# Performance work log

Hardware: AMD Instinct MI355X
Metric: run time of the kernel (lower is better)

The kernel has to match this reference:

```python
import jax, jax.numpy as jnp
import numpy as np

N_NODES = 100000


def setup_inputs() -> dict:
    key = jax.random.key(0)
    k1, k2, k3 = jax.random.split(key, 3)
    x = jax.random.normal(k1, (N_NODES, 256), dtype=jnp.float32)
    edge_index = jax.random.randint(k2, (2, 1600000), 0, N_NODES, dtype=jnp.int64)
    # GCNConv learned params (glorot weight, zero bias as in PyG init)
    W = jax.random.normal(k3, (256, 64), dtype=jnp.float32) * (1.0 / np.sqrt(256.0))
    b = jnp.zeros((64,), dtype=jnp.float32)
    return {"x": x, "edge_index": edge_index, "W": W, "b": b}


def reference(x, edge_index, W, b):
    n = x.shape[0]
    # --- gcn_norm: add self-loops, symmetric normalization ---
    loops = jnp.arange(n, dtype=edge_index.dtype)
    row = jnp.concatenate([edge_index[0], loops])  # source nodes
    col = jnp.concatenate([edge_index[1], loops])  # target nodes
    ones = jnp.ones(row.shape[0], dtype=x.dtype)
    deg = jax.ops.segment_sum(ones, col, num_segments=n)  # [N]
    dinv = jnp.where(deg > 0, jax.lax.rsqrt(deg), 0.0)
    norm = dinv[row] * dinv[col]  # [E+N]
    # --- linear transform then normalized scatter-add aggregation ---
    h = x @ W  # [N, out]
    msgs = h[row] * norm[:, None]  # [E+N, out]
    out = jax.ops.segment_sum(msgs, col, num_segments=n)  # [N, out]
    return out + b
```

## Files before the change

### kernel.cpp

```cpp
#include <hip/hip_runtime.h>


#define IN_F 256
#define OUT_F 64
#define WBITS 9
#define MAXBINS 256
#define CSHIFT 23
#define ROWMASK 0x7FFFFFu
#define CHUNK 4096

typedef unsigned short ushort_t;
typedef short bf16x8 __attribute__((ext_vector_type(8)));
typedef float f32x4 __attribute__((ext_vector_type(4)));

static __device__ __forceinline__ unsigned f2bf1(float f) {
    unsigned u = __float_as_uint(f);
    return (u + 0x7FFFu + ((u >> 16) & 1u)) >> 16;
}
static __device__ __forceinline__ unsigned pk2(float a, float b) {
    return f2bf1(a) | (f2bf1(b) << 16);
}
static __device__ __forceinline__ ushort_t f2bf(float f) { return (ushort_t)f2bf1(f); }
static __device__ __forceinline__ float bf2f(ushort_t h) {
    return __uint_as_float(((unsigned)h) << 16);
}

__global__ __launch_bounds__(256) void init_kernel(const float* __restrict__ W,
                                                   ushort_t* __restrict__ wfrag,
                                                   const int* __restrict__ col,
                                                   int* __restrict__ binCnt,
                                                   int* __restrict__ partialCnt,
                                                   int E, int nbins) {
    int gt = blockIdx.x * 256 + threadIdx.x;
    if (gt < 2048) {
        int t = gt;
        int kk = t >> 8;
        int ct = (t >> 6) & 3;
        int l  = t & 63;
        int k0 = kk * 32 + (l >> 4) * 8;
        int c  = ct * 16 + (l & 15);
        unsigned u0 = pk2(W[(k0 + 0) * OUT_F + c], W[(k0 + 1) * OUT_F + c]);
        unsigned u1 = pk2(W[(k0 + 2) * OUT_F + c], W[(k0 + 3) * OUT_F + c]);
        unsigned u2 = pk2(W[(k0 + 4) * OUT_F + c], W[(k0 + 5) * OUT_F + c]);
        unsigned u3 = pk2(W[(k0 + 6) * OUT_F + c], W[(k0 + 7) * OUT_F + c]);
        ((uint4*)wfrag)[t] = make_uint4(u0, u1, u2, u3);
    }
    __shared__ int hist[MAXBINS];
    int tid = threadIdx.x;
    if (tid < nbins) hist[tid] = 0;
    __syncthreads();
    int s = blockIdx.x * CHUNK;
    int epos = min(E, s + CHUNK);
    for (int e = s + tid; e < epos; e += 256)
        atomicAdd(&hist[col[e] >> WBITS], 1);
    __syncthreads();
    if (tid < nbins) {
        int c = hist[tid];
        partialCnt[blockIdx.x * MAXBINS + tid] = c;
        if (c) atomicAdd(&binCnt[tid], c);
    }
}

__global__ void bin_scan_kernel(const int* __restrict__ binCnt, int* __restrict__ binStart,
                                int* __restrict__ binCursor, int* __restrict__ start_n,
                                int nbins) {
    __shared__ int lds[MAXBINS];
    int tid = threadIdx.x;
    int v = (tid < nbins) ? binCnt[tid] : 0;
    lds[tid] = v;
    __syncthreads();
    for (int d = 1; d < MAXBINS; d <<= 1) {
        int t = (tid >= d) ? lds[tid - d] : 0;
        __syncthreads();
        lds[tid] += t;
        __syncthreads();
    }
    if (tid < nbins) {
        int ex = lds[tid] - v;
        binStart[tid] = ex;
        binCursor[tid] = ex;
    }
    if (tid == MAXBINS - 1) {
        binStart[nbins] = lds[MAXBINS - 1];
        start_n[0] = lds[MAXBINS - 1];
    }
}

__global__ __launch_bounds__(256) void mega_kernel(const float* __restrict__ x,
                                                   const ushort_t* __restrict__ wfrag,
                                                   ushort_t* __restrict__ h,
                                                   const int* __restrict__ row,
                                                   const int* __restrict__ col,
                                                   const int* __restrict__ partialCnt,
                                                   int* __restrict__ binCursor,
                                                   unsigned* __restrict__ ebuf,
                                                   int n, int E, int nbins, int gemmBlocks) {
    int tid = threadIdx.x;

    if (blockIdx.x < gemmBlocks) {
        int l  = tid & 63;
        int lr = l & 15;
        int lg = l >> 4;
        int rowbase = blockIdx.x * 64 + (tid >> 6) * 16;
        int arow = rowbase + lr;
        int lrow = (arow < n) ? arow : (n - 1);
        const float* xp = x + (size_t)lrow * IN_F + lg * 8;
        const uint4* wf = (const uint4*)wfrag;

        f32x4 acc0 = {0.f, 0.f, 0.f, 0.f};
        f32x4 acc1 = {0.f, 0.f, 0.f, 0.f};
        f32x4 acc2 = {0.f, 0.f, 0.f, 0.f};
        f32x4 acc3 = {0.f, 0.f, 0.f, 0.f};

        #pragma unroll
        for (int kk = 0; kk < 8; ++kk) {
            float4 xa = *(const float4*)(xp + kk * 32);
            float4 xb = *(const float4*)(xp + kk * 32 + 4);
            union { bf16x8 v; unsigned u[4]; } A;
            A.u[0] = pk2(xa.x, xa.y);
            A.u[1] = pk2(xa.z, xa.w);
            A.u[2] = pk2(xb.x, xb.y);
            A.u[3] = pk2(xb.z, xb.w);
            union { uint4 q; bf16x8 v; } B0, B1, B2, B3;
            B0.q = wf[(kk * 4 + 0) * 64 + l];
            B1.q = wf[(kk * 4 + 1) * 64 + l];
            B2.q = wf[(kk * 4 + 2) * 64 + l];
            B3.q = wf[(kk * 4 + 3) * 64 + l];
            acc0 = __builtin_amdgcn_mfma_f32_16x16x32_bf16(A.v, B0.v, acc0, 0, 0, 0);
            acc1 = __builtin_amdgcn_mfma_f32_16x16x32_bf16(A.v, B1.v, acc1, 0, 0, 0);
            acc2 = __builtin_amdgcn_mfma_f32_16x16x32_bf16(A.v, B2.v, acc2, 0, 0, 0);
            acc3 = __builtin_amdgcn_mfma_f32_16x16x32_bf16(A.v, B3.v, acc3, 0, 0, 0);
        }

        #pragma unroll
        for (int q = 0; q < 4; ++q) {
            int r = rowbase + lg * 4 + q;
            if (r < n) {
                ushort_t* gp = h + (size_t)r * OUT_F + lr;
                gp[0]  = f2bf(acc0[q]);
                gp[16] = f2bf(acc1[q]);
                gp[32] = f2bf(acc2[q]);
                gp[48] = f2bf(acc3[q]);
            }
        }
    } else {
        __shared__ int gbase[MAXBINS];
        __shared__ int lbase[MAXBINS];
        __shared__ int lcur[MAXBINS];
        __shared__ unsigned sorted[CHUNK];
        __shared__ int sdst[CHUNK];

        int sb = blockIdx.x - gemmBlocks;
        int s = sb * CHUNK;
        int epos = min(E, s + CHUNK);

        int c = (tid < nbins) ? partialCnt[sb * MAXBINS + tid] : 0;
        if (tid < nbins) gbase[tid] = c ? atomicAdd(&binCursor[tid], c) : 0;
        lbase[tid] = c;
        __syncthreads();
        for (int d = 1; d < MAXBINS; d <<= 1) {
            int t = (tid >= d) ? lbase[tid - d] : 0;
            __syncthreads();
            lbase[tid] += t;
            __syncthreads();
        }
        int ex = lbase[tid] - c;
        lbase[tid] = ex;
        lcur[tid] = ex;
        __syncthreads();

        for (int e = s + tid; e < epos; e += 256) {
            int cc = col[e];
            int bin = cc >> WBITS;
            int slot = atomicAdd(&lcur[bin], 1);
            sorted[slot] = (unsigned)row[e] | ((unsigned)(cc & ((1 << WBITS) - 1)) << CSHIFT);
            sdst[slot]   = gbase[bin] + (slot - lbase[bin]);
        }
        __syncthreads();

        int csize = epos - s;
        for (int i = tid; i < csize; i += 256)
            ebuf[sdst[i]] = sorted[i];
    }
}

__global__ __launch_bounds__(512) void fine_build_kernel(const unsigned* __restrict__ ebuf,
                                                         const int* __restrict__ binStart,
                                                         int* __restrict__ start,
                                                         float* __restrict__ dinv,
                                                         int* __restrict__ bucket, int n) {
    __shared__ int sdeg[512];
    __shared__ int scur[512];
    int b = blockIdx.x;
    int lo = b << WBITS;
    int wcnt = min(512, n - lo);
    int tid = threadIdx.x;
    sdeg[tid] = 0;
    __syncthreads();
    int s = binStart[b], epos = binStart[b + 1];
    for (int e = s + tid; e < epos; e += 512)
        atomicAdd(&sdeg[ebuf[e] >> CSHIFT], 1);
    __syncthreads();
    int d = sdeg[tid];
    if (tid < wcnt) dinv[lo + tid] = rsqrtf((float)(d + 1));
    for (int dd = 1; dd < 512; dd <<= 1) {
        int t = (tid >= dd) ? sdeg[tid - dd] : 0;
        __syncthreads();
        sdeg[tid] += t;
        __syncthreads();
    }
    int ex = sdeg[tid] - d;
    if (tid < wcnt) start[lo + tid] = s + ex;
    scur[tid] = ex;
    __syncthreads();
    for (int e = s + tid; e < epos; e += 512) {
        unsigned pr = ebuf[e];
        int pos = atomicAdd(&scur[pr >> CSHIFT], 1);
        bucket[s + pos] = (int)(pr & ROWMASK);
    }
}

__global__ __launch_bounds__(256) void gather_kernel(const int* __restrict__ start,
                              const int* __restrict__ bucket, const ushort_t* __restrict__ h,
                              const float* __restrict__ dinv, const float* __restrict__ b,
                              float* __restrict__ out, int n) {
    int lane = threadIdx.x & 63;
    int node = blockIdx.x * 4 + (threadIdx.x >> 6);
    if (node >= n) return;
    int f8  = lane & 7;
    int grp = lane >> 3;
    int s0  = start[node];
    int cnt = start[node + 1] - s0;
    const int* bp = bucket + s0;
    int last = cnt - 1;

    float a0 = 0.f, a1 = 0.f, a2 = 0.f, a3 = 0.f;
    float a4 = 0.f, a5 = 0.f, a6 = 0.f, a7 = 0.f;
    union { uint4 q; ushort_t s[8]; } VA, VB;
    for (int e0 = 0; e0 < cnt; e0 += 16) {
        int eA = e0 + grp;
        int eB = e0 + 8 + grp;
        int iA = bp[min(eA, last)];
        int iB = bp[min(eB, last)];
        VA.q = *(const uint4*)(h + (size_t)iA * OUT_F + f8 * 8);
        VB.q = *(const uint4*)(h + (size_t)iB * OUT_F + f8 * 8);
        float dA = (eA < cnt) ? dinv[iA] : 0.f;
        float dB = (eB < cnt) ? dinv[iB] : 0.f;
        a0 += bf2f(VA.s[0]) * dA;
        a1 += bf2f(VA.s[1]) * dA;
        a2 += bf2f(VA.s[2]) * dA;
        a3 += bf2f(VA.s[3]) * dA;
        a4 += bf2f(VA.s[4]) * dA;
        a5 += bf2f(VA.s[5]) * dA;
        a6 += bf2f(VA.s[6]) * dA;
        a7 += bf2f(VA.s[7]) * dA;
        a0 += bf2f(VB.s[0]) * dB;
        a1 += bf2f(VB.s[1]) * dB;
        a2 += bf2f(VB.s[2]) * dB;
        a3 += bf2f(VB.s[3]) * dB;
        a4 += bf2f(VB.s[4]) * dB;
        a5 += bf2f(VB.s[5]) * dB;
        a6 += bf2f(VB.s[6]) * dB;
        a7 += bf2f(VB.s[7]) * dB;
    }
    #pragma unroll
    for (int off = 8; off < 64; off <<= 1) {
        a0 += __shfl_xor(a0, off, 64);
        a1 += __shfl_xor(a1, off, 64);
        a2 += __shfl_xor(a2, off, 64);
        a3 += __shfl_xor(a3, off, 64);
        a4 += __shfl_xor(a4, off, 64);
        a5 += __shfl_xor(a5, off, 64);
        a6 += __shfl_xor(a6, off, 64);
        a7 += __shfl_xor(a7, off, 64);
    }

    if (grp == 0) {
        union { uint4 q; ushort_t s[8]; } SV;
        SV.q = *(const uint4*)(h + (size_t)node * OUT_F + f8 * 8);
        float dc = dinv[node];
        const float4* bv = (const float4*)b;
        float4 o0, o1;
        o0.x = (a0 + bf2f(SV.s[0]) * dc) * dc + bv[f8 * 2].x;
        o0.y = (a1 + bf2f(SV.s[1]) * dc) * dc + bv[f8 * 2].y;
        o0.z = (a2 + bf2f(SV.s[2]) * dc) * dc + bv[f8 * 2].z;
        o0.w = (a3 + bf2f(SV.s[3]) * dc) * dc + bv[f8 * 2].w;
        o1.x = (a4 + bf2f(SV.s[4]) * dc) * dc + bv[f8 * 2 + 1].x;
        o1.y = (a5 + bf2f(SV.s[5]) * dc) * dc + bv[f8 * 2 + 1].y;
        o1.z = (a6 + bf2f(SV.s[6]) * dc) * dc + bv[f8 * 2 + 1].z;
        o1.w = (a7 + bf2f(SV.s[7]) * dc) * dc + bv[f8 * 2 + 1].w;
        float4* op = (float4*)(out + (size_t)node * OUT_F + f8 * 8);
        op[0] = o0;
        op[1] = o1;
    }
}

extern "C" void kernel_launch(void* const* d_in, const int* in_sizes, int n_in,
                              void* d_out, int out_size, void* d_ws, size_t ws_size,
                              hipStream_t stream) {
    const float* x  = (const float*)d_in[0];
    const int*   ei = (const int*)d_in[1];
    const float* W  = (const float*)d_in[2];
    const float* b  = (const float*)d_in[3];
    float* out = (float*)d_out;

    int n = in_sizes[0] / IN_F;
    int E = in_sizes[1] / 2;
    const int* rowp = ei;
    const int* colp = ei + E;

    int nbins = (n + (1 << WBITS) - 1) >> WBITS;
    int SB = (E + CHUNK - 1) / CHUNK;

    char* wp = (char*)d_ws;
    ushort_t* h    = (ushort_t*)wp;
    unsigned* ebuf = (unsigned*)(wp + (size_t)n * OUT_F * 2);
    int* bucket    = (int*)(ebuf + E);
    ushort_t* wfrag = (ushort_t*)(bucket + E);
    int* start     = (int*)(wfrag + 16384);
    float* dinv    = (float*)(start + n + 1);
    int* binCnt    = (int*)(dinv + n);
    int* binStart  = binCnt + MAXBINS;
    int* binCursor = binStart + MAXBINS + 1;
    int* partialCnt= binCursor + MAXBINS;

    int gemmBlocks = (n + 63) / 64;

    hipMemsetAsync(binCnt, 0, MAXBINS * sizeof(int), stream);
    init_kernel<<<SB, 256, 0, stream>>>(W, wfrag, colp, binCnt, partialCnt, E, nbins);
    bin_scan_kernel<<<1, MAXBINS, 0, stream>>>(binCnt, binStart, binCursor, start + n, nbins);
    mega_kernel<<<gemmBlocks + SB, 256, 0, stream>>>(x, wfrag, h, rowp, colp,
                                                     partialCnt, binCursor, ebuf,
                                                     n, E, nbins, gemmBlocks);
    fine_build_kernel<<<nbins, 512, 0, stream>>>(ebuf, binStart, start, dinv, bucket, n);
    gather_kernel<<<(n + 3) / 4, 256, 0, stream>>>(start, bucket, h, dinv, b, out, n);
}
```

Before: 127.8 us.

## Pair GEMM with histogram pass and split scatter into its own kernel

The weight-fragment packing moves into a small standalone kernel. The GEMM blocks now share a launch with the column histogram instead of with the edge scatter, and the scatter runs as a separate kernel after the bin scan. The aim is to overlap the x@W GEMM with the lighter histogram pass and to give the scatter kernel leaner resources: its large LDS arrays are no longer shared with the GEMM code path, which may have limited occupancy. The cost is one extra kernel launch.

```diff
diff --git a/kernel.cpp b/kernel.cpp
--- a/kernel.cpp
+++ b/kernel.cpp
@@ -25,83 +25,52 @@
     return __uint_as_float(((unsigned)h) << 16);
 }
 
-__global__ __launch_bounds__(256) void init_kernel(const float* __restrict__ W,
-                                                   ushort_t* __restrict__ wfrag,
-                                                   const int* __restrict__ col,
-                                                   int* __restrict__ binCnt,
-                                                   int* __restrict__ partialCnt,
-                                                   int E, int nbins) {
-    int gt = blockIdx.x * 256 + threadIdx.x;
-    if (gt < 2048) {
-        int t = gt;
-        int kk = t >> 8;
-        int ct = (t >> 6) & 3;
-        int l  = t & 63;
-        int k0 = kk * 32 + (l >> 4) * 8;
-        int c  = ct * 16 + (l & 15);
-        unsigned u0 = pk2(W[(k0 + 0) * OUT_F + c], W[(k0 + 1) * OUT_F + c]);
-        unsigned u1 = pk2(W[(k0 + 2) * OUT_F + c], W[(k0 + 3) * OUT_F + c]);
-        unsigned u2 = pk2(W[(k0 + 4) * OUT_F + c], W[(k0 + 5) * OUT_F + c]);
-        unsigned u3 = pk2(W[(k0 + 6) * OUT_F + c], W[(k0 + 7) * OUT_F + c]);
-        ((uint4*)wfrag)[t] = make_uint4(u0, u1, u2, u3);
-    }
+__global__ void wfrag_kernel(const float* __restrict__ W, ushort_t* __restrict__ wfrag) {
+    int t = blockIdx.x * 256 + threadIdx.x;
+    if (t >= 2048) return;
+    int kk = t >> 8;
+    int ct = (t >> 6) & 3;
+    int l  = t & 63;
+    int k0 = kk * 32 + (l >> 4) * 8;
+    int c  = ct * 16 + (l & 15);
+    unsigned u0 = pk2(W[(k0 + 0) * OUT_F + c], W[(k0 + 1) * OUT_F + c]);
+    unsigned u1 = pk2(W[(k0 + 2) * OUT_F + c], W[(k0 + 3) * OUT_F + c]);
+    unsigned u2 = pk2(W[(k0 + 4) * OUT_F + c], W[(k0 + 5) * OUT_F + c]);
+    unsigned u3 = pk2(W[(k0 + 6) * OUT_F + c], W[(k0 + 7) * OUT_F + c]);
+    ((uint4*)wfrag)[t] = make_uint4(u0, u1, u2, u3);
+}
+
+__global__ __launch_bounds__(256) void gemm_hist_kernel(const float* __restrict__ x,
+                                                        const ushort_t* __restrict__ wfrag,
+                                                        ushort_t* __restrict__ h,
+                                                        const int* __restrict__ col,
+                                                        int* __restrict__ binCnt,
+                                                        int* __restrict__ partialCnt,
+                                                        int n, int E, int nbins, int SB) {
     __shared__ int hist[MAXBINS];
     int tid = threadIdx.x;
-    if (tid < nbins) hist[tid] = 0;
-    __syncthreads();
-    int s = blockIdx.x * CHUNK;
-    int epos = min(E, s + CHUNK);
-    for (int e = s + tid; e < epos; e += 256)
-        atomicAdd(&hist[col[e] >> WBITS], 1);
-    __syncthreads();
-    if (tid < nbins) {
-        int c = hist[tid];
-        partialCnt[blockIdx.x * MAXBINS + tid] = c;
-        if (c) atomicAdd(&binCnt[tid], c);
-    }
-}
-
-__global__ void bin_scan_kernel(const int* __restrict__ binCnt, int* __restrict__ binStart,
-                                int* __restrict__ binCursor, int* __restrict__ start_n,
-                                int nbins) {
-    __shared__ int lds[MAXBINS];
-    int tid = threadIdx.x;
-    int v = (tid < nbins) ? binCnt[tid] : 0;
-    lds[tid] = v;
-    __syncthreads();
-    for (int d = 1; d < MAXBINS; d <<= 1) {
-        int t = (tid >= d) ? lds[tid - d] : 0;
-        __syncthreads();
-        lds[tid] += t;
-        __syncthreads();
-    }
-    if (tid < nbins) {
-        int ex = lds[tid] - v;
-        binStart[tid] = ex;
-        binCursor[tid] = ex;
-    }
-    if (tid == MAXBINS - 1) {
-        binStart[nbins] = lds[MAXBINS - 1];
-        start_n[0] = lds[MAXBINS - 1];
-    }
-}
-
-__global__ __launch_bounds__(256) void mega_kernel(const float* __restrict__ x,
-                                                   const ushort_t* __restrict__ wfrag,
-                                                   ushort_t* __restrict__ h,
-                                                   const int* __restrict__ row,
-                                                   const int* __restrict__ col,
-                                                   const int* __restrict__ partialCnt,
-                                                   int* __restrict__ binCursor,
-                                                   unsigned* __restrict__ ebuf,
-                                                   int n, int E, int nbins, int gemmBlocks) {
-    int tid = threadIdx.x;
-
-    if (blockIdx.x < gemmBlocks) {
+
+    if (blockIdx.x < SB) {
+        int sb = blockIdx.x;
+        if (tid < nbins) hist[tid] = 0;
+        __syncthreads();
+        int s = sb * CHUNK;
+        int epos = min(E, s + CHUNK);
+        for (int e = s + tid; e < epos; e += 256)
+            atomicAdd(&hist[col[e] >> WBITS], 1);
+        __syncthreads();
+        if (tid < nbins) {
+            int c = hist[tid];
+            partialCnt[sb * MAXBINS + tid] = c;
+            if (c) atomicAdd(&binCnt[tid], c);
+        }
+    } else {
+        int gb = blockIdx.x - SB;
         int l  = tid & 63;
         int lr = l & 15;
         int lg = l >> 4;
-        int rowbase = blockIdx.x * 64 + (tid >> 6) * 16;
+        int rowbase = gb * 64 + (tid >> 6) * 16;
+        if (rowbase >= n) return;
         int arow = rowbase + lr;
         int lrow = (arow < n) ? arow : (n - 1);
         const float* xp = x + (size_t)lrow * IN_F + lg * 8;
@@ -143,45 +112,78 @@
                 gp[48] = f2bf(acc3[q]);
             }
         }
-    } else {
-        __shared__ int gbase[MAXBINS];
-        __shared__ int lbase[MAXBINS];
-        __shared__ int lcur[MAXBINS];
-        __shared__ unsigned sorted[CHUNK];
-        __shared__ int sdst[CHUNK];
-
-        int sb = blockIdx.x - gemmBlocks;
-        int s = sb * CHUNK;
-        int epos = min(E, s + CHUNK);
-
-        int c = (tid < nbins) ? partialCnt[sb * MAXBINS + tid] : 0;
-        if (tid < nbins) gbase[tid] = c ? atomicAdd(&binCursor[tid], c) : 0;
-        lbase[tid] = c;
-        __syncthreads();
-        for (int d = 1; d < MAXBINS; d <<= 1) {
-            int t = (tid >= d) ? lbase[tid - d] : 0;
-            __syncthreads();
-            lbase[tid] += t;
-            __syncthreads();
-        }
-        int ex = lbase[tid] - c;
-        lbase[tid] = ex;
-        lcur[tid] = ex;
-        __syncthreads();
-
-        for (int e = s + tid; e < epos; e += 256) {
-            int cc = col[e];
-            int bin = cc >> WBITS;
-            int slot = atomicAdd(&lcur[bin], 1);
-            sorted[slot] = (unsigned)row[e] | ((unsigned)(cc & ((1 << WBITS) - 1)) << CSHIFT);
-            sdst[slot]   = gbase[bin] + (slot - lbase[bin]);
-        }
-        __syncthreads();
-
-        int csize = epos - s;
-        for (int i = tid; i < csize; i += 256)
-            ebuf[sdst[i]] = sorted[i];
-    }
+    }
+}
+
+__global__ void bin_scan_kernel(const int* __restrict__ binCnt, int* __restrict__ binStart,
+                                int* __restrict__ binCursor, int* __restrict__ start_n,
+                                int nbins) {
+    __shared__ int lds[MAXBINS];
+    int tid = threadIdx.x;
+    int v = (tid < nbins) ? binCnt[tid] : 0;
+    lds[tid] = v;
+    __syncthreads();
+    for (int d = 1; d < MAXBINS; d <<= 1) {
+        int t = (tid >= d) ? lds[tid - d] : 0;
+        __syncthreads();
+        lds[tid] += t;
+        __syncthreads();
+    }
+    if (tid < nbins) {
+        int ex = lds[tid] - v;
+        binStart[tid] = ex;
+        binCursor[tid] = ex;
+    }
+    if (tid == MAXBINS - 1) {
+        binStart[nbins] = lds[MAXBINS - 1];
+        start_n[0] = lds[MAXBINS - 1];
+    }
+}
+
+__global__ __launch_bounds__(256) void scatter_kernel(const int* __restrict__ row,
+                                                      const int* __restrict__ col,
+                                                      const int* __restrict__ partialCnt,
+                                                      int* __restrict__ binCursor,
+                                                      unsigned* __restrict__ ebuf,
+                                                      int E, int nbins) {
+    __shared__ int gbase[MAXBINS];
+    __shared__ int lbase[MAXBINS];
+    __shared__ int lcur[MAXBINS];
+    __shared__ unsigned sorted[CHUNK];
+    __shared__ int sdst[CHUNK];
+
+    int tid = threadIdx.x;
+    int sb = blockIdx.x;
+    int s = sb * CHUNK;
+    int epos = min(E, s + CHUNK);
+
+    int c = (tid < nbins) ? partialCnt[sb * MAXBINS + tid] : 0;
+    if (tid < nbins) gbase[tid] = c ? atomicAdd(&binCursor[tid], c) : 0;
+    lbase[tid] = c;
+    __syncthreads();
+    for (int d = 1; d < MAXBINS; d <<= 1) {
+        int t = (tid >= d) ? lbase[tid - d] : 0;
+        __syncthreads();
+        lbase[tid] += t;
+        __syncthreads();
+    }
+    int ex = lbase[tid] - c;
+    lbase[tid] = ex;
+    lcur[tid] = ex;
+    __syncthreads();
+
+    for (int e = s + tid; e < epos; e += 256) {
+        int cc = col[e];
+        int bin = cc >> WBITS;
+        int slot = atomicAdd(&lcur[bin], 1);
+        sorted[slot] = (unsigned)row[e] | ((unsigned)(cc & ((1 << WBITS) - 1)) << CSHIFT);
+        sdst[slot]   = gbase[bin] + (slot - lbase[bin]);
+    }
+    __syncthreads();
+
+    int csize = epos - s;
+    for (int i = tid; i < csize; i += 256)
+        ebuf[sdst[i]] = sorted[i];
 }
 
 __global__ __launch_bounds__(512) void fine_build_kernel(const unsigned* __restrict__ ebuf,
@@ -327,11 +329,11 @@
     int gemmBlocks = (n + 63) / 64;
 
     hipMemsetAsync(binCnt, 0, MAXBINS * sizeof(int), stream);
-    init_kernel<<<SB, 256, 0, stream>>>(W, wfrag, colp, binCnt, partialCnt, E, nbins);
+    wfrag_kernel<<<8, 256, 0, stream>>>(W, wfrag);
+    gemm_hist_kernel<<<SB + gemmBlocks, 256, 0, stream>>>(x, wfrag, h, colp, binCnt,
+                                                          partialCnt, n, E, nbins, SB);
     bin_scan_kernel<<<1, MAXBINS, 0, stream>>>(binCnt, binStart, binCursor, start + n, nbins);
-    mega_kernel<<<gemmBlocks + SB, 256, 0, stream>>>(x, wfrag, h, rowp, colp,
-                                                     partialCnt, binCursor, ebuf,
-                                                     n, E, nbins, gemmBlocks);
+    scatter_kernel<<<SB, 256, 0, stream>>>(rowp, colp, partialCnt, binCursor, ebuf, E, nbins);
     fine_build_kernel<<<nbins, 512, 0, stream>>>(ebuf, binStart, start, dinv, bucket, n);
     gather_kernel<<<(n + 3) / 4, 256, 0, stream>>>(start, bucket, h, dinv, b, out, n);
 }
```

Measured after the change: 131.2 us. +2.6%, slower.
